# Kernel tuning notes

Hardware: AMD Instinct MI355X
Metric: run time of the kernel (lower is better)

## Reference

```python
import jax, jax.numpy as jnp
import numpy as np

IN_CH = 4096
OUT_CH = 4096
DENSITY = 0.1
BATCH = 8192


def setup_inputs() -> dict:
    key = jax.random.key(0)
    k_mask, k_w, k_b, k_x = jax.random.split(key, 4)
    # Fixed sparsity pattern, as in the torch module's sparse_mask.nonzero()
    mask = jax.random.bernoulli(k_mask, DENSITY, (OUT_CH, IN_CH))
    rows, cols = jnp.nonzero(mask)  # unique (row, col) pairs
    rows = rows.astype(jnp.int32)
    cols = cols.astype(jnp.int32)
    nnz = rows.shape[0]
    # Kaiming-style init per output row (approximate: uniform bound from mean fan-in)
    fan_in = jnp.maximum(jnp.sum(mask, axis=1).astype(jnp.float32), 1.0)  # [OUT_CH]
    gain = np.sqrt(2.0 / (1.0 + 5.0))  # leaky_relu gain with a=sqrt(5)
    std = gain / jnp.sqrt(fan_in)
    w_bound = np.sqrt(3.0) * std  # per-row bound
    u = jax.random.uniform(k_w, (nnz,), minval=-1.0, maxval=1.0)
    sparse_weight = u * w_bound[rows]
    b_bound = 1.0 / jnp.sqrt(fan_in)
    bias = jax.random.uniform(k_b, (OUT_CH,), minval=-1.0, maxval=1.0) * b_bound
    x = jax.random.normal(k_x, (BATCH, IN_CH), dtype=jnp.float32)
    return {
        "x": x,
        "sparse_weight": sparse_weight.astype(jnp.float32),
        "rows": rows,
        "cols": cols,
        "bias": bias.astype(jnp.float32),
    }


def reference(x, sparse_weight, rows, cols, bias):
    # Rebuild the (fixed-pattern) sparse weight as a dense [OUT_CH, IN_CH] matrix
    # (indices are unique, so .set matches the COO semantics), then y = x @ W^T + b.
    W = jnp.zeros((OUT_CH, IN_CH), dtype=sparse_weight.dtype).at[rows, cols].set(sparse_weight)
    return x @ W.T + bias  # [BATCH, OUT_CH]
```

## Files before the change

### kernel.cpp

```cpp
#include <hip/hip_runtime.h>
#include <hip/hip_bf16.h>

#define M_DIM 8192
#define N_DIM 4096
#define K_DIM 4096
#define BM 128
#define BN 128
#define BK 32

typedef __bf16 bf16x8 __attribute__((ext_vector_type(8)));
typedef float  f32x4  __attribute__((ext_vector_type(4)));
typedef unsigned short u16x8 __attribute__((ext_vector_type(8)));

#define ASYNC16(g, l)                                                          \
  __builtin_amdgcn_global_load_lds(                                            \
      (__attribute__((address_space(1))) void*)(g),                            \
      (__attribute__((address_space(3))) void*)(l), 16, 0, 0)

static __device__ __forceinline__ unsigned short f2bf(float f) {
  unsigned int u = __float_as_uint(f);
  u += 0x7fffu + ((u >> 16) & 1u);
  return (unsigned short)(u >> 16);
}

__global__ void sl_cvt_bf16(const float4* __restrict__ x4, u16x8* __restrict__ xb,
                            int n8) {
  int i = blockIdx.x * 256 + threadIdx.x;
  if (i >= n8) return;
  float4 a = x4[2 * i];
  float4 b = x4[2 * i + 1];
  u16x8 o;
  o[0] = f2bf(a.x); o[1] = f2bf(a.y); o[2] = f2bf(a.z); o[3] = f2bf(a.w);
  o[4] = f2bf(b.x); o[5] = f2bf(b.y); o[6] = f2bf(b.z); o[7] = f2bf(b.w);
  xb[i] = o;
}

__global__ void sl_scatter(const float* __restrict__ vals, const int* __restrict__ rows,
                           const int* __restrict__ cols, unsigned short* __restrict__ W,
                           int nnz) {
  int k = blockIdx.x * 256 + threadIdx.x;
  if (k >= nnz) return;
  W[(size_t)rows[k] * K_DIM + cols[k]] = f2bf(vals[k]);
}

__global__ __launch_bounds__(256) void sl_gemm_bias(
    const unsigned short* __restrict__ A,
    const unsigned short* __restrict__ B,
    const float* __restrict__ bias,
    float* __restrict__ C) {
  __shared__ __align__(16) unsigned short As[BM * BK];
  __shared__ __align__(16) unsigned short Bs[BN * BK];

  const int tid  = threadIdx.x;
  const int wave = tid >> 6;
  const int lane = tid & 63;
  const int m0 = blockIdx.x * BM;
  const int n0 = blockIdx.y * BN;

  const int srow = tid >> 2;
  const int scol = (tid & 3) * 8;
  const unsigned short* gA0 = A + (size_t)(m0 + srow) * K_DIM + scol;
  const unsigned short* gA1 = gA0 + (size_t)64 * K_DIM;
  const unsigned short* gB0 = B + (size_t)(n0 + srow) * K_DIM + scol;
  const unsigned short* gB1 = gB0 + (size_t)64 * K_DIM;
  unsigned short* lA0 = As + (size_t)(wave * 64) * 8;
  unsigned short* lA1 = As + (size_t)(256 + wave * 64) * 8;
  unsigned short* lB0 = Bs + (size_t)(wave * 64) * 8;
  unsigned short* lB1 = Bs + (size_t)(256 + wave * 64) * 8;

  const int wm   = (wave >> 1) * 64;
  const int wn   = (wave & 1) * 64;
  const int fm   = lane & 15;
  const int quad = lane >> 4;

  f32x4 acc[4][4] = {};

  for (int k0 = 0; k0 < K_DIM; k0 += BK) {
    ASYNC16(gA0, lA0);
    ASYNC16(gA1, lA1);
    ASYNC16(gB0, lB0);
    ASYNC16(gB1, lB1);
    gA0 += BK; gA1 += BK; gB0 += BK; gB1 += BK;
    __syncthreads();

    bf16x8 af[4], bfr[4];
#pragma unroll
    for (int t = 0; t < 4; ++t) {
      af[t]  = *(const bf16x8*)(As + (size_t)(wm + t * 16 + fm) * BK + quad * 8);
      bfr[t] = *(const bf16x8*)(Bs + (size_t)(wn + t * 16 + fm) * BK + quad * 8);
    }
#pragma unroll
    for (int tm = 0; tm < 4; ++tm)
#pragma unroll
      for (int tn = 0; tn < 4; ++tn)
        acc[tm][tn] = __builtin_amdgcn_mfma_f32_16x16x32_bf16(
            af[tm], bfr[tn], acc[tm][tn], 0, 0, 0);
    __syncthreads();
  }

  float bv[4];
#pragma unroll
  for (int tn = 0; tn < 4; ++tn) bv[tn] = bias[n0 + wn + tn * 16 + fm];

#pragma unroll
  for (int tm = 0; tm < 4; ++tm) {
    const int mbase = m0 + wm + tm * 16 + quad * 4;
#pragma unroll
    for (int tn = 0; tn < 4; ++tn) {
      const int n = n0 + wn + tn * 16 + fm;
      float* p = C + (size_t)mbase * N_DIM + n;
#pragma unroll
      for (int r = 0; r < 4; ++r)
        p[(size_t)r * N_DIM] = acc[tm][tn][r] + bv[tn];
    }
  }
}

__global__ void sl_naive(const float* __restrict__ x, const float* __restrict__ vals,
                         const int* __restrict__ rows, const int* __restrict__ cols,
                         const float* __restrict__ bias, float* __restrict__ out,
                         int nnz) {
  const int o = blockIdx.x;
  int l = 0, h = nnz;
  while (l < h) { int m = (l + h) >> 1; if (rows[m] < o) l = m + 1; else h = m; }
  const int s = l;
  h = nnz;
  while (l < h) { int m = (l + h) >> 1; if (rows[m] <= o) l = m + 1; else h = m; }
  const int e = l;
  const float bv = bias[o];
  for (int b = threadIdx.x; b < M_DIM; b += blockDim.x) {
    float acc = bv;
    const float* xb = x + (size_t)b * K_DIM;
    for (int k = s; k < e; ++k) acc += vals[k] * xb[cols[k]];
    out[(size_t)b * N_DIM + o] = acc;
  }
}

extern "C" void kernel_launch(void* const* d_in, const int* in_sizes, int n_in,
                              void* d_out, int out_size, void* d_ws, size_t ws_size,
                              hipStream_t stream) {
  const float* x    = (const float*)d_in[0];
  const float* vals = (const float*)d_in[1];
  const int*   rows = (const int*)d_in[2];
  const int*   cols = (const int*)d_in[3];
  const float* bias = (const float*)d_in[4];
  float* out = (float*)d_out;
  const int nnz = in_sizes[1];

  const size_t xb_bytes = (size_t)M_DIM * K_DIM * 2;
  const size_t w_bytes  = (size_t)N_DIM * K_DIM * 2;

  if (ws_size >= xb_bytes + w_bytes) {
    unsigned short* xb = (unsigned short*)d_ws;
    unsigned short* W  = (unsigned short*)((char*)d_ws + xb_bytes);

    hipMemsetAsync(W, 0, w_bytes, stream);
    const int n8 = (M_DIM * K_DIM) / 8;
    sl_cvt_bf16<<<(n8 + 255) / 256, 256, 0, stream>>>((const float4*)x, (u16x8*)xb, n8);
    sl_scatter<<<(nnz + 255) / 256, 256, 0, stream>>>(vals, rows, cols, W, nnz);
    sl_gemm_bias<<<dim3(M_DIM / BM, N_DIM / BN), 256, 0, stream>>>(xb, W, bias, out);
  } else {
    sl_naive<<<N_DIM, 256, 0, stream>>>(x, vals, rows, cols, bias, out, nnz);
  }
}
```

Measured before the change: 541.2 us.

## Fuse weight densify and input conversion into one kernel; swizzle LDS layout

```diff
diff --git a/kernel.cpp b/kernel.cpp
--- a/kernel.cpp
+++ b/kernel.cpp
@@ -23,24 +23,39 @@
   return (unsigned short)(u >> 16);
 }
 
-__global__ void sl_cvt_bf16(const float4* __restrict__ x4, u16x8* __restrict__ xb,
-                            int n8) {
-  int i = blockIdx.x * 256 + threadIdx.x;
-  if (i >= n8) return;
-  float4 a = x4[2 * i];
-  float4 b = x4[2 * i + 1];
-  u16x8 o;
-  o[0] = f2bf(a.x); o[1] = f2bf(a.y); o[2] = f2bf(a.z); o[3] = f2bf(a.w);
-  o[4] = f2bf(b.x); o[5] = f2bf(b.y); o[6] = f2bf(b.z); o[7] = f2bf(b.w);
-  xb[i] = o;
-}
-
-__global__ void sl_scatter(const float* __restrict__ vals, const int* __restrict__ rows,
-                           const int* __restrict__ cols, unsigned short* __restrict__ W,
-                           int nnz) {
-  int k = blockIdx.x * 256 + threadIdx.x;
-  if (k >= nnz) return;
-  W[(size_t)rows[k] * K_DIM + cols[k]] = f2bf(vals[k]);
+__global__ __launch_bounds__(256) void sl_prep(
+    const float4* __restrict__ x4, u16x8* __restrict__ xb,
+    const float* __restrict__ vals, const int* __restrict__ rows,
+    const int* __restrict__ cols, unsigned short* __restrict__ W, int nnz) {
+  const int b = blockIdx.x;
+  if (b < N_DIM) {
+    __shared__ __align__(16) unsigned short rowbuf[K_DIM];
+    u16x8* rb8 = (u16x8*)rowbuf;
+    u16x8 z = {};
+    rb8[threadIdx.x] = z;
+    rb8[256 + threadIdx.x] = z;
+    __syncthreads();
+    int l = 0, h = nnz;
+    while (l < h) { int m = (l + h) >> 1; if (rows[m] < b) l = m + 1; else h = m; }
+    const int s = l;
+    h = nnz;
+    while (l < h) { int m = (l + h) >> 1; if (rows[m] <= b) l = m + 1; else h = m; }
+    const int e = l;
+    for (int k = s + threadIdx.x; k < e; k += 256)
+      rowbuf[cols[k]] = f2bf(vals[k]);
+    __syncthreads();
+    u16x8* dst = (u16x8*)(W + (size_t)b * K_DIM);
+    dst[threadIdx.x] = rb8[threadIdx.x];
+    dst[256 + threadIdx.x] = rb8[256 + threadIdx.x];
+  } else {
+    const int i = (b - N_DIM) * 256 + threadIdx.x;
+    float4 a = x4[2 * i];
+    float4 c = x4[2 * i + 1];
+    u16x8 o;
+    o[0] = f2bf(a.x); o[1] = f2bf(a.y); o[2] = f2bf(a.z); o[3] = f2bf(a.w);
+    o[4] = f2bf(c.x); o[5] = f2bf(c.y); o[6] = f2bf(c.z); o[7] = f2bf(c.w);
+    xb[i] = o;
+  }
 }
 
 __global__ __launch_bounds__(256) void sl_gemm_bias(
@@ -58,7 +73,7 @@
   const int n0 = blockIdx.y * BN;
 
   const int srow = tid >> 2;
-  const int scol = (tid & 3) * 8;
+  const int scol = ((tid & 3) ^ ((tid >> 3) & 3)) * 8;
   const unsigned short* gA0 = A + (size_t)(m0 + srow) * K_DIM + scol;
   const unsigned short* gA1 = gA0 + (size_t)64 * K_DIM;
   const unsigned short* gB0 = B + (size_t)(n0 + srow) * K_DIM + scol;
@@ -72,6 +87,8 @@
   const int wn   = (wave & 1) * 64;
   const int fm   = lane & 15;
   const int quad = lane >> 4;
+  const int sw   = (fm >> 1) & 3;
+  const int kc   = (quad ^ sw) * 8;
 
   f32x4 acc[4][4] = {};
 
@@ -86,8 +103,8 @@
     bf16x8 af[4], bfr[4];
 #pragma unroll
     for (int t = 0; t < 4; ++t) {
-      af[t]  = *(const bf16x8*)(As + (size_t)(wm + t * 16 + fm) * BK + quad * 8);
-      bfr[t] = *(const bf16x8*)(Bs + (size_t)(wn + t * 16 + fm) * BK + quad * 8);
+      af[t]  = *(const bf16x8*)(As + (size_t)(wm + t * 16 + fm) * BK + kc);
+      bfr[t] = *(const bf16x8*)(Bs + (size_t)(wn + t * 16 + fm) * BK + kc);
     }
 #pragma unroll
     for (int tm = 0; tm < 4; ++tm)
@@ -154,10 +171,9 @@
     unsigned short* xb = (unsigned short*)d_ws;
     unsigned short* W  = (unsigned short*)((char*)d_ws + xb_bytes);
 
-    hipMemsetAsync(W, 0, w_bytes, stream);
-    const int n8 = (M_DIM * K_DIM) / 8;
-    sl_cvt_bf16<<<(n8 + 255) / 256, 256, 0, stream>>>((const float4*)x, (u16x8*)xb, n8);
-    sl_scatter<<<(nnz + 255) / 256, 256, 0, stream>>>(vals, rows, cols, W, nnz);
+    const int cvt_blocks = (M_DIM * K_DIM) / 8 / 256;
+    sl_prep<<<N_DIM + cvt_blocks, 256, 0, stream>>>(
+        (const float4*)x, (u16x8*)xb, vals, rows, cols, W, nnz);
     sl_gemm_bias<<<dim3(M_DIM / BM, N_DIM / BN), 256, 0, stream>>>(xb, W, bias, out);
   } else {
     sl_naive<<<N_DIM, 256, 0, stream>>>(x, vals, rows, cols, bias, out, nnz);
```

Result: slower. 561.4 us (+3.7%).
